# Kernel tuning notes

Measured on AMD Instinct MI355X. Metric: run time of the kernel, lower is better.

The kernel has to match this reference:

```python
import jax, jax.numpy as jnp
import numpy as np

B, DIM, HEADS, H, W = 2, 256, 8, 40, 40


def setup_inputs() -> dict:
    key = jax.random.key(0)
    ks = jax.random.split(key, 11)
    s = 0.05
    return {
        "x": jax.random.normal(ks[0], (B, DIM, H, W), jnp.float32),
        "qkv_w": jax.random.normal(ks[1], (3 * DIM, DIM, 1, 1), jnp.float32) * s,
        "qkv_b": jax.random.normal(ks[2], (3 * DIM,), jnp.float32) * s,
        "pos_w": jax.random.normal(ks[3], (3 * DIM, 1, 3, 3), jnp.float32) * s,
        "pos_b": jax.random.normal(ks[4], (3 * DIM,), jnp.float32) * s,
        "proj_w": jax.random.normal(ks[5], (DIM, DIM), jnp.float32) * s,
        "proj_b": jax.random.normal(ks[6], (DIM,), jnp.float32) * s,
        "g1_w": jax.random.normal(ks[7], (16, 1), jnp.float32),
        "g1_b": jax.random.normal(ks[8], (16,), jnp.float32),
        "g2_w": jax.random.normal(ks[9], (1, 16), jnp.float32),
        "g2_b": jax.random.normal(ks[10], (1,), jnp.float32),
    }


def _conv(x, w, b, groups=1, pad=0):
    # NCHW conv, OIHW weights (matches torch Conv2d)
    y = jax.lax.conv_general_dilated(x, w, (1, 1), [(pad, pad), (pad, pad)],
                                     feature_group_count=groups)
    return y + b[None, :, None, None]


def reference(x, qkv_w, qkv_b, pos_w, pos_b, proj_w, proj_b, g1_w, g1_b, g2_w, g2_b):
    b, c, h, w = x.shape
    n = h * w
    hd = c // HEADS
    scale = hd ** -0.5

    qkv = _conv(x, qkv_w, qkv_b)                     # [b, 3c, h, w]
    qkv = _conv(qkv, pos_w, pos_b, groups=3 * c, pad=1)  # depthwise 3x3
    q, k, v = jnp.split(qkv, 3, axis=1)

    def to_heads(t):  # [b,c,h,w] -> [b, heads, n, head_dim]
        return t.reshape(b, HEADS, hd, n).transpose(0, 1, 3, 2)

    q, k, v = to_heads(q), to_heads(k), to_heads(v)

    attn = jnp.einsum('bhnd,bhmd->bhnm', q, k) * scale      # [b,H,n,n]
    prob = jax.nn.softmax(attn, axis=-1)
    entropy = -(prob * jnp.log(jnp.clip(prob, 1e-12))).sum(-1).mean(-1)  # [b,H]

    # EntropyGate: ratio in [0.1, 1.0]
    hid = jax.nn.relu(entropy[..., None] @ g1_w.T + g1_b)
    ratio = jax.nn.sigmoid(hid @ g2_w.T + g2_b)[..., 0] * 0.9 + 0.1      # [b,H]

    # dynamic per-(b,head) top-k: keep = ceil(ratio*n), clamped to [1,n]
    keep = jnp.clip(jnp.ceil(ratio * n).astype(jnp.int32), 1, n)          # [b,H]
    srt = jnp.flip(jnp.sort(attn, axis=-1), axis=-1)                      # descending
    idx = jnp.broadcast_to((keep - 1)[:, :, None, None], (b, HEADS, n, 1))
    kth = jnp.take_along_axis(srt, idx, axis=-1)                          # [b,H,n,1]
    sparse = jnp.where(attn >= kth, attn, -jnp.inf)

    p = jax.nn.softmax(sparse, axis=-1)
    out = jnp.einsum('bhnm,bhmd->bhnd', p, v)
    out = out.transpose(0, 2, 1, 3).reshape(b, n, c)
    out = out @ proj_w.T + proj_b
    return out.transpose(0, 2, 1).reshape(b, c, h, w)
```

## Files before the change

### kernel.cpp

```cpp
#include <hip/hip_runtime.h>
#include <math.h>

#define BB 2
#define CDIM 256
#define NHEADS 8
#define HD 32
#define HH 40
#define WW 40
#define NN 1600
#define C3 768
#define SCALE 0.17677669529663687f
#define RTE 8
#define RTS 2
#define TSTR 2048
#define HSTR 51200

typedef __attribute__((ext_vector_type(4))) float f4;

__device__ inline unsigned fkey(float f) {
    unsigned u = __float_as_uint(f);
    return (u & 0x80000000u) ? ~u : (u | 0x80000000u);
}
__device__ inline float finv(unsigned u) {
    unsigned v = (u & 0x80000000u) ? (u ^ 0x80000000u) : ~u;
    return __uint_as_float(v);
}

__global__ __launch_bounds__(256) void conv1x1_kernel(const float* __restrict__ x,
                                                      const float* __restrict__ w,
                                                      const float* __restrict__ bias,
                                                      float* __restrict__ out) {
    int blk = blockIdx.x;
    int st = blk % 7;
    int t2 = blk / 7;
    int ocg = t2 % (C3 / 8);
    int b = t2 / (C3 / 8);
    int s = st * 256 + threadIdx.x;
    if (s >= NN) return;
    int oc0 = ocg * 8;
    const float* xb = x + (size_t)b * CDIM * NN + s;
    const float* w0 = w + (size_t)oc0 * CDIM;
    float a[8];
#pragma unroll
    for (int i = 0; i < 8; i++) a[i] = bias[oc0 + i];
#pragma unroll 4
    for (int ic = 0; ic < CDIM; ic++) {
        float xv = xb[(size_t)ic * NN];
#pragma unroll
        for (int i = 0; i < 8; i++) a[i] += w0[i * CDIM + ic] * xv;
    }
    float* ob = out + ((size_t)b * C3 + oc0) * NN + s;
#pragma unroll
    for (int i = 0; i < 8; i++) ob[(size_t)i * NN] = a[i];
}

__global__ __launch_bounds__(256) void dwconv_kernel(const float* __restrict__ in,
                                                     const float* __restrict__ w,
                                                     const float* __restrict__ bias,
                                                     float* __restrict__ out_t) {
    int idx = blockIdx.x * 256 + threadIdx.x;
    int s = idx % NN;
    int t = idx / NN;
    int c = t % C3;
    int b = t / C3;
    int y = s / WW, xx = s % WW;
    const float* ib = in + ((size_t)b * C3 + c) * NN;
    const float* wr = w + (size_t)c * 9;
    float acc = bias[c];
#pragma unroll
    for (int ky = 0; ky < 3; ky++) {
        int iy = y + ky - 1;
        if (iy < 0 || iy >= HH) continue;
#pragma unroll
        for (int kx = 0; kx < 3; kx++) {
            int ix = xx + kx - 1;
            if (ix < 0 || ix >= WW) continue;
            acc += wr[ky * 3 + kx] * ib[iy * WW + ix];
        }
    }
    int part = c >> 8;
    int r = c & 255;
    int hh = r >> 5;
    int d = r & 31;
    out_t[((size_t)(b * 3 + part) * NHEADS + hh) * HSTR + (s >> 6) * TSTR + d * 64 + (s & 63)] = acc;
}

template <int PERSIST>
__global__ __launch_bounds__(256) void entropy_kernel(const float* __restrict__ qkv_t,
                                                      float* __restrict__ ent,
                                                      float* __restrict__ attw) {
    int blk = blockIdx.x;
    int rt = blk % (NN / RTE);
    int bh = blk / (NN / RTE);
    int h = bh % NHEADS, b = bh / NHEADS;
    int row0 = rt * RTE;
    __shared__ float Qs[RTE][HD];
    int tid = threadIdx.x;
    const float* qt = qkv_t + ((size_t)(b * 3 + 0) * NHEADS + h) * HSTR;
    const float* ktb = qkv_t + ((size_t)(b * 3 + 1) * NHEADS + h) * HSTR;
    {
        int r = tid >> 5, d = tid & 31;
        int row = row0 + r;
        Qs[r][d] = qt[(row >> 6) * TSTR + d * 64 + (row & 63)];
    }
    __syncthreads();
    int w = tid >> 6, lane = tid & 63;
    int lr0 = 2 * w, lr1 = lr0 + 1;
    float* aw0 = nullptr;
    float* aw1 = nullptr;
    if (PERSIST) {
        aw0 = attw + ((size_t)bh * NN + row0 + lr0) * NN;
        aw1 = aw0 + NN;
    }
    float q0[HD], q1[HD];
#pragma unroll
    for (int d = 0; d < HD; d++) { q0[d] = Qs[lr0][d]; q1[d] = Qs[lr1][d]; }
    float S0 = 0.f, T0 = 0.f, S1 = 0.f, T1 = 0.f;
#pragma unroll 1
    for (int kt = 0; kt < 25; kt++) {
        const float* kp = ktb + kt * TSTR + lane;
        float a0 = 0.f, a1 = 0.f;
#pragma unroll
        for (int dc = 0; dc < 4; dc++) {
            float kc[8];
#pragma unroll
            for (int i = 0; i < 8; i++) kc[i] = kp[(dc * 8 + i) * 64];
#pragma unroll
            for (int i = 0; i < 8; i++) {
                a0 += q0[dc * 8 + i] * kc[i];
                a1 += q1[dc * 8 + i] * kc[i];
            }
        }
        a0 *= SCALE; a1 *= SCALE;
        if (PERSIST) {
            int j = kt * 64 + lane;
            aw0[j] = a0;
            aw1[j] = a1;
        }
        float e0 = __expf(a0), e1 = __expf(a1);
        S0 += e0; T0 += e0 * a0;
        S1 += e1; T1 += e1 * a1;
    }
#pragma unroll
    for (int o = 1; o < 64; o <<= 1) {
        S0 += __shfl_xor(S0, o); T0 += __shfl_xor(T0, o);
        S1 += __shfl_xor(S1, o); T1 += __shfl_xor(T1, o);
    }
    if (lane == 0) {
        ent[(size_t)bh * NN + row0 + lr0] = logf(S0) - T0 / S0;
        ent[(size_t)bh * NN + row0 + lr1] = logf(S1) - T1 / S1;
    }
}

__global__ void gate_kernel(const float* __restrict__ ent_rows,
                            const float* __restrict__ g1w, const float* __restrict__ g1b,
                            const float* __restrict__ g2w, const float* __restrict__ g2b,
                            int* __restrict__ keep) {
    int bh = blockIdx.x;
    int tid = threadIdx.x;
    __shared__ float red[4];
    float ls = 0.f;
    for (int j = tid; j < NN; j += 256) ls += ent_rows[bh * NN + j];
    for (int o = 32; o > 0; o >>= 1) ls += __shfl_down(ls, o);
    int lane = tid & 63, wid = tid >> 6;
    if (lane == 0) red[wid] = ls;
    __syncthreads();
    if (tid == 0) {
        float ent = (red[0] + red[1] + red[2] + red[3]) / (float)NN;
        float val = g2b[0];
#pragma unroll
        for (int j = 0; j < 16; j++) {
            float hid = ent * g1w[j] + g1b[j];
            if (hid < 0.f) hid = 0.f;
            val += hid * g2w[j];
        }
        float ratio = 0.9f / (1.f + expf(-val)) + 0.1f;
        int kp = (int)ceilf(ratio * (float)NN);
        if (kp < 1) kp = 1;
        if (kp > NN) kp = NN;
        keep[bh] = kp;
    }
}

__global__ __launch_bounds__(256, 4) void select_kernel(const float* __restrict__ attbuf,
                                                        const int* __restrict__ keep,
                                                        float* __restrict__ kth_out,
                                                        float* __restrict__ m_out) {
    int blk = blockIdx.x;
    int rt = blk % (NN / 8);
    int bh = blk / (NN / 8);
    int row0 = rt * 8;
    __shared__ unsigned hist[4][RTS][256];
    int tid = threadIdx.x;
    int wv = tid >> 6;
    int lane = tid & 63;
    int wrow0 = row0 + 2 * wv;
    int want = keep[bh];
    int l = lane & 31;
    int r = (lane < 32) ? 0 : 1;
    const float* ar = attbuf + ((size_t)bh * NN + wrow0 + r) * NN;

    unsigned kvr[50];
#pragma unroll
    for (int k2 = 0; k2 < 50; k2++) kvr[k2] = fkey(ar[k2 * 32 + l]);

    unsigned mk = 0u;
#pragma unroll
    for (int k2 = 0; k2 < 50; k2++) mk = mk > kvr[k2] ? mk : kvr[k2];
#pragma unroll
    for (int off = 1; off < 32; off <<= 1) {
        unsigned o = (unsigned)__shfl_xor((int)mk, off);
        mk = mk > o ? mk : o;
    }

    unsigned prefixHigh = 0;
    for (int pass = 0; pass < 4; pass++) {
        int shift = 24 - 8 * pass;
#pragma unroll
        for (int i = 0; i < 8; i++) hist[wv][r][248 - 8 * l + i] = 0u;
#pragma unroll
        for (int k2 = 0; k2 < 50; k2++) {
            unsigned u = kvr[k2];
            bool ok = (pass == 0) || ((u >> (shift + 8)) == prefixHigh);
            if (ok) atomicAdd(&hist[wv][r][(u >> shift) & 255u], 1u);
        }
        unsigned sch = 0;
#pragma unroll
        for (int i = 0; i < 8; i++) sch += hist[wv][r][248 - 8 * l + i];
        unsigned inc = sch;
#pragma unroll
        for (int dlt = 1; dlt < 32; dlt <<= 1) {
            unsigned tv = __shfl_up(inc, dlt, 32);
            if (l >= dlt) inc += tv;
        }
        unsigned pref = inc - sch;
        bool found = (pref < (unsigned)want) && ((unsigned)want <= inc);
        int bsel = -1, wnew = 0;
        if (found) {
            unsigned want2 = (unsigned)want - pref, cum = 0;
#pragma unroll
            for (int i = 0; i < 8; i++) {
                int bbin = 255 - 8 * l - i;
                unsigned c = hist[wv][r][bbin];
                if (bsel < 0 && cum + c >= want2) { bsel = bbin; wnew = (int)(want2 - cum); }
                cum += c;
            }
        }
        unsigned long long mkb = __ballot(found);
        int src = (lane < 32) ? __builtin_ctzll(mkb & 0xffffffffULL)
                              : __builtin_ctzll(mkb >> 32) + 32;
        bsel = __shfl(bsel, src);
        want = __shfl(wnew, src);
        prefixHigh = (prefixHigh << 8) | (unsigned)bsel;
    }
    if (l == 0) {
        kth_out[(size_t)bh * NN + wrow0 + r] = finv(prefixHigh);
        m_out[(size_t)bh * NN + wrow0 + r] = finv(mk);
    }
}

__global__ __launch_bounds__(256, 4) void pv_kernel(const float* __restrict__ qkv_t,
                                                    const float* __restrict__ attbuf,
                                                    const float* __restrict__ kth_in,
                                                    const float* __restrict__ m_in,
                                                    float* __restrict__ oht) {
    int blk = blockIdx.x;
    int rt = blk % (NN / 8);
    int bh = blk / (NN / 8);
    int h = bh % NHEADS, b = bh / NHEADS;
    int row0 = rt * 8;
    __shared__ float lds[4224];
    int tid = threadIdx.x;
    int wv = tid >> 6;
    int lane = tid & 63;
    int r0 = row0 + 2 * wv;
    const float* vtb = qkv_t + ((size_t)(b * 3 + 2) * NHEADS + h) * HSTR;
    const float* ab0 = attbuf + ((size_t)bh * NN + r0) * NN;
    const float* ab1 = ab0 + NN;
    float m0 = m_in[(size_t)bh * NN + r0];
    float m1 = m_in[(size_t)bh * NN + r0 + 1];
    float kth0 = kth_in[(size_t)bh * NN + r0];
    float kth1 = kth_in[(size_t)bh * NN + r0 + 1];

    float acc0[HD], acc1[HD];
#pragma unroll
    for (int d = 0; d < HD; d++) { acc0[d] = 0.f; acc1[d] = 0.f; }
    float S0 = 0.f, S1 = 0.f;

    f4 st0, st1;
    {
        const f4* vp = (const f4*)vtb;
        st0 = vp[tid];
        st1 = vp[256 + tid];
    }
    int cur = 0;
#pragma unroll 1
    for (int kt = 0; kt < 25; kt++) {
        {
            f4* dst = (f4*)&lds[cur * 2048];
            dst[tid] = st0;
            dst[256 + tid] = st1;
        }
        __syncthreads();
        if (kt + 1 < 25) {
            const f4* vp = (const f4*)(vtb + (kt + 1) * TSTR);
            st0 = vp[tid];
            st1 = vp[256 + tid];
        }
        const float* vb = &lds[cur * 2048];
        int j = kt * 64 + lane;
        float a0 = ab0[j];
        float a1 = ab1[j];
        float p0 = (a0 >= kth0) ? __expf(a0 - m0) : 0.f;
        float p1 = (a1 >= kth1) ? __expf(a1 - m1) : 0.f;
        S0 += p0; S1 += p1;
#pragma unroll
        for (int d = 0; d < HD; d++) {
            float vv = vb[d * 64 + lane];
            acc0[d] += p0 * vv;
            acc1[d] += p1 * vv;
        }
        cur ^= 1;
    }
#pragma unroll
    for (int off = 1; off < 64; off <<= 1) {
        S0 += __shfl_xor(S0, off);
        S1 += __shfl_xor(S1, off);
    }

#pragma unroll
    for (int d = 0; d < HD; d++) {
        acc0[d] += __shfl_xor(acc0[d], 32);
        acc1[d] += __shfl_xor(acc1[d], 32);
    }
    __syncthreads();
    float* sc = &lds[wv * 1056];
    int dd = lane & 31;
    if (lane < 32) {
#pragma unroll
        for (int d = 0; d < HD; d++) sc[lane * 33 + d] = acc0[d];
    }
    float sum0 = 0.f;
#pragma unroll
    for (int jj = 0; jj < 32; jj++) sum0 += sc[jj * 33 + dd];
    if (lane < 32) {
#pragma unroll
        for (int d = 0; d < HD; d++) sc[lane * 33 + d] = acc1[d];
    }
    float sum1 = 0.f;
#pragma unroll
    for (int jj = 0; jj < 32; jj++) sum1 += sc[jj * 33 + dd];

    if (lane < 32) {
        size_t base = ((size_t)b * CDIM + h * HD + dd) * NN + r0;
        oht[base + 0] = sum0 / S0;
        oht[base + 1] = sum1 / S1;
    }
}

__global__ __launch_bounds__(64) void sparse_attn_kernel(const float* __restrict__ qkv_t,
                                                         const int* __restrict__ keep,
                                                         float* __restrict__ oht) {
    int blk = blockIdx.x;
    int rt = blk % (NN / RTS);
    int bh = blk / (NN / RTS);
    int h = bh % NHEADS, b = bh / NHEADS;
    int row0 = rt * RTS;
    __shared__ float att[RTS][NN];
    __shared__ unsigned hist[RTS][256];
    __shared__ float Qs[RTS][HD];
    int tid = threadIdx.x;
    const float* qt = qkv_t + ((size_t)(b * 3 + 0) * NHEADS + h) * HSTR;
    const float* ktb = qkv_t + ((size_t)(b * 3 + 1) * NHEADS + h) * HSTR;
    const float* vtb = qkv_t + ((size_t)(b * 3 + 2) * NHEADS + h) * HSTR;
    {
        int r = tid >> 5, d = tid & 31;
        int row = row0 + r;
        Qs[r][d] = qt[(row >> 6) * TSTR + d * 64 + (row & 63)];
    }
    int want = keep[bh];
    __syncthreads();
    int lane = tid;
    float q0[HD], q1[HD];
#pragma unroll
    for (int d = 0; d < HD; d++) { q0[d] = Qs[0][d]; q1[d] = Qs[1][d]; }
    float m0 = -1e30f, m1 = -1e30f;
    for (int kt = 0; kt < 25; kt++) {
        const float* kp = ktb + kt * TSTR + lane;
        int j = kt * 64 + lane;
        float kc[HD];
#pragma unroll
        for (int d = 0; d < HD; d++) kc[d] = kp[d * 64];
        float a0 = 0.f, a1 = 0.f;
#pragma unroll
        for (int d = 0; d < HD; d++) { a0 += q0[d] * kc[d]; a1 += q1[d] * kc[d]; }
        a0 *= SCALE; a1 *= SCALE;
        att[0][j] = a0;
        att[1][j] = a1;
        m0 = fmaxf(m0, a0); m1 = fmaxf(m1, a1);
    }
#pragma unroll
    for (int off = 1; off < 64; off <<= 1) {
        m0 = fmaxf(m0, __shfl_xor(m0, off));
        m1 = fmaxf(m1, __shfl_xor(m1, off));
    }
    int l = lane & 31;
    int r = (lane < 32) ? 0 : 1;
    unsigned kvr[50];
#pragma unroll
    for (int k2 = 0; k2 < 50; k2++) kvr[k2] = fkey(att[r][k2 * 32 + l]);
    unsigned prefixHigh = 0;
    for (int pass = 0; pass < 4; pass++) {
        int shift = 24 - 8 * pass;
#pragma unroll
        for (int i = 0; i < 8; i++) hist[r][248 - 8 * l + i] = 0u;
#pragma unroll
        for (int k2 = 0; k2 < 50; k2++) {
            unsigned u = kvr[k2];
            bool ok = (pass == 0) || ((u >> (shift + 8)) == prefixHigh);
            if (ok) atomicAdd(&hist[r][(u >> shift) & 255u], 1u);
        }
        unsigned sch = 0;
#pragma unroll
        for (int i = 0; i < 8; i++) sch += hist[r][248 - 8 * l + i];
        unsigned inc = sch;
#pragma unroll
        for (int dlt = 1; dlt < 32; dlt <<= 1) {
            unsigned tv = __shfl_up(inc, dlt, 32);
            if (l >= dlt) inc += tv;
        }
        unsigned pref = inc - sch;
        bool found = (pref < (unsigned)want) && ((unsigned)want <= inc);
        int bsel = -1, wnew = 0;
        if (found) {
            unsigned want2 = (unsigned)want - pref, cum = 0;
#pragma unroll
            for (int i = 0; i < 8; i++) {
                int bbin = 255 - 8 * l - i;
                unsigned c = hist[r][bbin];
                if (bsel < 0 && cum + c >= want2) { bsel = bbin; wnew = (int)(want2 - cum); }
                cum += c;
            }
        }
        unsigned long long mk = __ballot(found);
        int src = (lane < 32) ? __builtin_ctzll(mk & 0xffffffffULL)
                              : __builtin_ctzll(mk >> 32) + 32;
        bsel = __shfl(bsel, src);
        want = __shfl(wnew, src);
        prefixHigh = (prefixHigh << 8) | (unsigned)bsel;
    }
    float kth = finv(prefixHigh);
    float kth0 = __shfl(kth, 0);
    float kth1 = __shfl(kth, 32);
    float acc0[HD], acc1[HD];
#pragma unroll
    for (int d = 0; d < HD; d++) { acc0[d] = 0.f; acc1[d] = 0.f; }
    float S0 = 0.f, S1 = 0.f;
    for (int kt = 0; kt < 25; kt++) {
        const float* vp = vtb + kt * TSTR + lane;
        int j = kt * 64 + lane;
        float a0 = att[0][j];
        float a1 = att[1][j];
        float p0 = (a0 >= kth0) ? __expf(a0 - m0) : 0.f;
        float p1 = (a1 >= kth1) ? __expf(a1 - m1) : 0.f;
        S0 += p0; S1 += p1;
#pragma unroll
        for (int d = 0; d < HD; d++) {
            float vv = vp[d * 64];
            acc0[d] += p0 * vv;
            acc1[d] += p1 * vv;
        }
    }
#pragma unroll
    for (int off = 1; off < 64; off <<= 1) {
        S0 += __shfl_xor(S0, off);
        S1 += __shfl_xor(S1, off);
    }
    float* scratch = &att[0][0];
    int dd = lane & 31;
    int jb = (lane < 32) ? 0 : 32;
#pragma unroll
    for (int d = 0; d < HD; d++) scratch[lane * 33 + d] = acc0[d];
    float sum0 = 0.f;
#pragma unroll
    for (int jj = 0; jj < 32; jj++) sum0 += scratch[(jb + jj) * 33 + dd];
    sum0 += __shfl_xor(sum0, 32);
#pragma unroll
    for (int d = 0; d < HD; d++) scratch[lane * 33 + d] = acc1[d];
    float sum1 = 0.f;
#pragma unroll
    for (int jj = 0; jj < 32; jj++) sum1 += scratch[(jb + jj) * 33 + dd];
    sum1 += __shfl_xor(sum1, 32);
    if (lane < 32) {
        size_t base = ((size_t)b * CDIM + h * HD + dd) * NN + row0;
        oht[base + 0] = sum0 / S0;
        oht[base + 1] = sum1 / S1;
    }
}

__global__ __launch_bounds__(256) void proj_kernel(const float* __restrict__ oht,
                                                   const float* __restrict__ pw,
                                                   const float* __restrict__ pb,
                                                   float* __restrict__ out) {
    int blk = blockIdx.x;
    int st = blk % 7;
    int t2 = blk / 7;
    int ocg = t2 % (CDIM / 8);
    int b = t2 / (CDIM / 8);
    int s = st * 256 + threadIdx.x;
    if (s >= NN) return;
    int co0 = ocg * 8;
    const float* ib = oht + (size_t)b * CDIM * NN + s;
    const float* w0 = pw + (size_t)co0 * CDIM;
    float a[8];
#pragma unroll
    for (int i = 0; i < 8; i++) a[i] = pb[co0 + i];
#pragma unroll 4
    for (int c = 0; c < CDIM; c++) {
        float xv = ib[(size_t)c * NN];
#pragma unroll
        for (int i = 0; i < 8; i++) a[i] += w0[i * CDIM + c] * xv;
    }
    float* ob = out + ((size_t)b * CDIM + co0) * NN + s;
#pragma unroll
    for (int i = 0; i < 8; i++) ob[(size_t)i * NN] = a[i];
}

extern "C" void kernel_launch(void* const* d_in, const int* in_sizes, int n_in,
                              void* d_out, int out_size, void* d_ws, size_t ws_size,
                              hipStream_t stream) {
    const float* x      = (const float*)d_in[0];
    const float* qkv_w  = (const float*)d_in[1];
    const float* qkv_b  = (const float*)d_in[2];
    const float* pos_w  = (const float*)d_in[3];
    const float* pos_b  = (const float*)d_in[4];
    const float* proj_w = (const float*)d_in[5];
    const float* proj_b = (const float*)d_in[6];
    const float* g1w    = (const float*)d_in[7];
    const float* g1b    = (const float*)d_in[8];
    const float* g2w    = (const float*)d_in[9];
    const float* g2b    = (const float*)d_in[10];
    float* out = (float*)d_out;

    float* ws   = (float*)d_ws;
    float* buf1 = ws;
    float* buf2 = buf1 + (size_t)BB * C3 * NN;
    float* ent  = buf2 + (size_t)BB * C3 * NN;
    float* oht  = ent + (size_t)BB * NHEADS * NN;
    int* keep   = (int*)(oht + (size_t)BB * CDIM * NN);
    float* kth  = (float*)(keep + 16);
    float* mrow = kth + (size_t)BB * NHEADS * NN;
    float* attbuf = mrow + (size_t)BB * NHEADS * NN;
    size_t need = (size_t)((char*)(attbuf + (size_t)BB * NHEADS * NN * NN) - (char*)d_ws);
    bool persist = (ws_size >= need);

    conv1x1_kernel<<<BB * (C3 / 8) * 7, 256, 0, stream>>>(x, qkv_w, qkv_b, buf1);
    dwconv_kernel<<<BB * C3 * NN / 256, 256, 0, stream>>>(buf1, pos_w, pos_b, buf2);
    if (persist) {
        entropy_kernel<1><<<NHEADS * BB * (NN / RTE), 256, 0, stream>>>(buf2, ent, attbuf);
        gate_kernel<<<BB * NHEADS, 256, 0, stream>>>(ent, g1w, g1b, g2w, g2b, keep);
        select_kernel<<<NHEADS * BB * (NN / 8), 256, 0, stream>>>(attbuf, keep, kth, mrow);
        pv_kernel<<<NHEADS * BB * (NN / 8), 256, 0, stream>>>(buf2, attbuf, kth, mrow, oht);
    } else {
        entropy_kernel<0><<<NHEADS * BB * (NN / RTE), 256, 0, stream>>>(buf2, ent, nullptr);
        gate_kernel<<<BB * NHEADS, 256, 0, stream>>>(ent, g1w, g1b, g2w, g2b, keep);
        sparse_attn_kernel<<<NHEADS * BB * (NN / RTS), 64, 0, stream>>>(buf2, keep, oht);
    }
    proj_kernel<<<BB * (CDIM / 8) * 7, 256, 0, stream>>>(oht, proj_w, proj_b, out);
}
```

Measured before the change: 414.1 us.

## Fuse top-k selection and PV accumulation into one kernel with LDS-staged rows

Merges select_kernel and pv_kernel into a single kernel. Each block stages its 8 attention rows (about 51 KB) into shared memory once. The radix threshold selection and the masked softmax-times-V accumulation both read from that copy, so the attention rows are read from global memory once instead of twice. This also drops the kth and row-max intermediate buffers and one launch. The cost is much larger LDS use per block (about 76 KB), which lowers occupancy, and the launch bound no longer requests 4 blocks per SM.

```diff
diff --git a/kernel.cpp b/kernel.cpp
--- a/kernel.cpp
+++ b/kernel.cpp
@@ -182,27 +182,37 @@
     }
 }
 
-__global__ __launch_bounds__(256, 4) void select_kernel(const float* __restrict__ attbuf,
+__global__ __launch_bounds__(256) void select_pv_kernel(const float* __restrict__ qkv_t,
+                                                        const float* __restrict__ attbuf,
                                                         const int* __restrict__ keep,
-                                                        float* __restrict__ kth_out,
-                                                        float* __restrict__ m_out) {
+                                                        float* __restrict__ oht) {
     int blk = blockIdx.x;
     int rt = blk % (NN / 8);
     int bh = blk / (NN / 8);
+    int h = bh % NHEADS, b = bh / NHEADS;
     int row0 = rt * 8;
-    __shared__ unsigned hist[4][RTS][256];
+    __shared__ float att[8][NN];
+    __shared__ unsigned hist[4][2][256];
+    __shared__ float vbuf[2][2048];
     int tid = threadIdx.x;
     int wv = tid >> 6;
     int lane = tid & 63;
-    int wrow0 = row0 + 2 * wv;
+    const float* vtb = qkv_t + ((size_t)(b * 3 + 2) * NHEADS + h) * HSTR;
+
+    {
+        const f4* ap = (const f4*)(attbuf + ((size_t)bh * NN + row0) * NN);
+        f4* al = (f4*)&att[0][0];
+        for (int i = tid; i < 3200; i += 256) al[i] = ap[i];
+    }
     int want = keep[bh];
+    __syncthreads();
+
     int l = lane & 31;
     int r = (lane < 32) ? 0 : 1;
-    const float* ar = attbuf + ((size_t)bh * NN + wrow0 + r) * NN;
-
+    int rowsel = 2 * wv + r;
     unsigned kvr[50];
 #pragma unroll
-    for (int k2 = 0; k2 < 50; k2++) kvr[k2] = fkey(ar[k2 * 32 + l]);
+    for (int k2 = 0; k2 < 50; k2++) kvr[k2] = fkey(att[rowsel][k2 * 32 + l]);
 
     unsigned mk = 0u;
 #pragma unroll
@@ -212,6 +222,9 @@
         unsigned o = (unsigned)__shfl_xor((int)mk, off);
         mk = mk > o ? mk : o;
     }
+    float mhalf = finv(mk);
+    float m0 = __shfl(mhalf, 0);
+    float m1 = __shfl(mhalf, 32);
 
     unsigned prefixHigh = 0;
     for (int pass = 0; pass < 4; pass++) {
@@ -253,40 +266,14 @@
         want = __shfl(wnew, src);
         prefixHigh = (prefixHigh << 8) | (unsigned)bsel;
     }
-    if (l == 0) {
-        kth_out[(size_t)bh * NN + wrow0 + r] = finv(prefixHigh);
-        m_out[(size_t)bh * NN + wrow0 + r] = finv(mk);
-    }
-}
-
-__global__ __launch_bounds__(256, 4) void pv_kernel(const float* __restrict__ qkv_t,
-                                                    const float* __restrict__ attbuf,
-                                                    const float* __restrict__ kth_in,
-                                                    const float* __restrict__ m_in,
-                                                    float* __restrict__ oht) {
-    int blk = blockIdx.x;
-    int rt = blk % (NN / 8);
-    int bh = blk / (NN / 8);
-    int h = bh % NHEADS, b = bh / NHEADS;
-    int row0 = rt * 8;
-    __shared__ float lds[4224];
-    int tid = threadIdx.x;
-    int wv = tid >> 6;
-    int lane = tid & 63;
-    int r0 = row0 + 2 * wv;
-    const float* vtb = qkv_t + ((size_t)(b * 3 + 2) * NHEADS + h) * HSTR;
-    const float* ab0 = attbuf + ((size_t)bh * NN + r0) * NN;
-    const float* ab1 = ab0 + NN;
-    float m0 = m_in[(size_t)bh * NN + r0];
-    float m1 = m_in[(size_t)bh * NN + r0 + 1];
-    float kth0 = kth_in[(size_t)bh * NN + r0];
-    float kth1 = kth_in[(size_t)bh * NN + r0 + 1];
+    float kth = finv(prefixHigh);
+    float kth0 = __shfl(kth, 0);
+    float kth1 = __shfl(kth, 32);
 
     float acc0[HD], acc1[HD];
 #pragma unroll
     for (int d = 0; d < HD; d++) { acc0[d] = 0.f; acc1[d] = 0.f; }
     float S0 = 0.f, S1 = 0.f;
-
     f4 st0, st1;
     {
         const f4* vp = (const f4*)vtb;
@@ -297,7 +284,7 @@
 #pragma unroll 1
     for (int kt = 0; kt < 25; kt++) {
         {
-            f4* dst = (f4*)&lds[cur * 2048];
+            f4* dst = (f4*)&vbuf[cur][0];
             dst[tid] = st0;
             dst[256 + tid] = st1;
         }
@@ -307,10 +294,10 @@
             st0 = vp[tid];
             st1 = vp[256 + tid];
         }
-        const float* vb = &lds[cur * 2048];
+        const float* vb = &vbuf[cur][0];
         int j = kt * 64 + lane;
-        float a0 = ab0[j];
-        float a1 = ab1[j];
+        float a0 = att[2 * wv][j];
+        float a1 = att[2 * wv + 1][j];
         float p0 = (a0 >= kth0) ? __expf(a0 - m0) : 0.f;
         float p1 = (a1 >= kth1) ? __expf(a1 - m1) : 0.f;
         S0 += p0; S1 += p1;
@@ -333,8 +320,7 @@
         acc0[d] += __shfl_xor(acc0[d], 32);
         acc1[d] += __shfl_xor(acc1[d], 32);
     }
-    __syncthreads();
-    float* sc = &lds[wv * 1056];
+    float* sc = &att[2 * wv][0];
     int dd = lane & 31;
     if (lane < 32) {
 #pragma unroll
@@ -352,6 +338,7 @@
     for (int jj = 0; jj < 32; jj++) sum1 += sc[jj * 33 + dd];
 
     if (lane < 32) {
+        int r0 = row0 + 2 * wv;
         size_t base = ((size_t)b * CDIM + h * HD + dd) * NN + r0;
         oht[base + 0] = sum0 / S0;
         oht[base + 1] = sum1 / S1;
@@ -548,9 +535,7 @@
     float* ent  = buf2 + (size_t)BB * C3 * NN;
     float* oht  = ent + (size_t)BB * NHEADS * NN;
     int* keep   = (int*)(oht + (size_t)BB * CDIM * NN);
-    float* kth  = (float*)(keep + 16);
-    float* mrow = kth + (size_t)BB * NHEADS * NN;
-    float* attbuf = mrow + (size_t)BB * NHEADS * NN;
+    float* attbuf = (float*)(keep + 16);
     size_t need = (size_t)((char*)(attbuf + (size_t)BB * NHEADS * NN * NN) - (char*)d_ws);
     bool persist = (ws_size >= need);
 
@@ -559,8 +544,7 @@
     if (persist) {
         entropy_kernel<1><<<NHEADS * BB * (NN / RTE), 256, 0, stream>>>(buf2, ent, attbuf);
         gate_kernel<<<BB * NHEADS, 256, 0, stream>>>(ent, g1w, g1b, g2w, g2b, keep);
-        select_kernel<<<NHEADS * BB * (NN / 8), 256, 0, stream>>>(attbuf, keep, kth, mrow);
-        pv_kernel<<<NHEADS * BB * (NN / 8), 256, 0, stream>>>(buf2, attbuf, kth, mrow, oht);
+        select_pv_kernel<<<NHEADS * BB * (NN / 8), 256, 0, stream>>>(buf2, attbuf, keep, oht);
     } else {
         entropy_kernel<0><<<NHEADS * BB * (NN / RTE), 256, 0, stream>>>(buf2, ent, nullptr);
         gate_kernel<<<BB * NHEADS, 256, 0, stream>>>(ent, g1w, g1b, g2w, g2b, keep);
```

Result: slower. 460.8 us (+11.3%).
